# Kernel optimization log

Measured on AMD Instinct MI355X. Metric: run time of the kernel, lower is better.

Reference implementation:

```python
import jax, jax.numpy as jnp
import numpy as np

EPS = 1e-5

def _conv3x3(x, w, b):
    # x: (B,C,H,W), w: (O,I,3,3) OIHW, SAME padding, stride 1
    y = jax.lax.conv_general_dilated(x, w, (1, 1), 'SAME',
                                     dimension_numbers=('NCHW', 'OIHW', 'NCHW'))
    return y + b[None, :, None, None]

def _inorm(x):
    # InstanceNorm2d (affine=False, eval-free): per-sample per-channel over HW
    m = jnp.mean(x, axis=(2, 3), keepdims=True)
    v = jnp.var(x, axis=(2, 3), keepdims=True)
    return (x - m) * jax.lax.rsqrt(v + EPS)

def _pac_conv_transpose(x, guide, w, b, stride=2, padding=1, out_pad=1):
    # PacConvTranspose2d (gaussian kernel, not channel-wise, unnormalized):
    # 1) zero-stuff input by stride, pad by (k-1)-padding (+output_padding on the
    #    bottom/right), 2) run a 3x3 conv whose taps are modulated per-pixel by
    #    K_ij = exp(-0.5 * ||g(p+ij) - g(p)||^2) computed from the guidance map.
    # w: (Cin, Cout, k, k)  (torch transposed-conv layout)
    k = w.shape[2]
    B, C, H, Wd = x.shape
    xs = jnp.zeros((B, C, (H - 1) * stride + 1, (Wd - 1) * stride + 1), x.dtype)
    xs = xs.at[:, :, ::stride, ::stride].set(x)
    p = (k - 1) - padding
    xp = jnp.pad(xs, ((0, 0), (0, 0), (p, p + out_pad), (p, p + out_pad)))
    gpad = (k - 1) // 2
    gp = jnp.pad(guide, ((0, 0), (0, 0), (gpad, gpad), (gpad, gpad)))
    Ho, Wo = guide.shape[2], guide.shape[3]
    out = jnp.zeros((B, w.shape[1], Ho, Wo), x.dtype)
    for i in range(k):          # fixed 3x3 tap loop (not a data-dim loop)
        for j in range(k):
            gn = gp[:, :, i:i + Ho, j:j + Wo]
            kk = jnp.exp(-0.5 * jnp.sum((gn - guide) ** 2, axis=1, keepdims=True))  # (B,1,Ho,Wo)
            xn = xp[:, :, i:i + Ho, j:j + Wo]                                        # (B,Cin,Ho,Wo)
            out = out + jnp.einsum('bchw,co->bohw', xn * kk, w[:, :, i, j])
    return out + b[None, :, None, None]

def setup_inputs() -> dict:
    key = jax.random.key(0)
    ks = jax.random.split(key, 16)
    C = 64
    s = 0.02  # small weight scale to keep gaussian adaptive kernels well-conditioned
    inp = {
        'x':      jax.random.normal(ks[0], (1, 4 * C, 64, 64), jnp.float32),
        'ef_lv2': jax.random.normal(ks[1], (1, 2 * C, 128, 128), jnp.float32),
        'ef_lv1': jax.random.normal(ks[2], (1, C, 256, 256), jnp.float32),
        'w_adj2': jax.random.normal(ks[3], (4 * C, 2 * C, 3, 3), jnp.float32) * s,
        'b_adj2': jnp.zeros((4 * C,), jnp.float32),
        'w_adj1': jax.random.normal(ks[4], (2 * C, C, 3, 3), jnp.float32) * s,
        'b_adj1': jnp.zeros((2 * C,), jnp.float32),
        'w_pac16': jax.random.normal(ks[5], (4 * C, 2 * C, 3, 3), jnp.float32) * s,
        'b_pac16': jnp.zeros((2 * C,), jnp.float32),
        'w_pac20': jax.random.normal(ks[6], (2 * C, C, 3, 3), jnp.float32) * s,
        'b_pac20': jnp.zeros((C,), jnp.float32),
        'w_out':  jax.random.normal(ks[7], (3, C, 3, 3), jnp.float32) * s,
        'b_out':  jnp.zeros((3,), jnp.float32),
    }
    return inp

def reference(x, ef_lv2, ef_lv1, w_adj2, b_adj2, w_adj1, b_adj1,
              w_pac16, b_pac16, w_pac20, b_pac20, w_out, b_out):
    x = _inorm(x) + x                       # layer13 + residual
    x = _inorm(x) + x                       # layer14 + residual
    g2 = _conv3x3(ef_lv2, w_adj2, b_adj2)   # adjust_ef_lv2_pacconv
    x = _pac_conv_transpose(x, g2, w_pac16, b_pac16)  # layer16: 64->128
    x = _inorm(x) + x                       # layer17
    x = _inorm(x) + x                       # layer18
    g1 = _conv3x3(ef_lv1, w_adj1, b_adj1)   # adjust_ef_lv1_pacconv
    x = _pac_conv_transpose(x, g1, w_pac20, b_pac20)  # layer20: 128->256
    x = _inorm(x) + x                       # layer21
    x = _inorm(x) + x                       # layer22
    return _conv3x3(x, w_out, b_out)        # layer24 -> (B,3,256,256)
```

## Files before the change

### kernel.cpp

```cpp
#include <hip/hip_runtime.h>
#include <hip/hip_bf16.h>
#include <cstdint>
#include <cstddef>

#define EPS_IN 1e-5f

typedef __attribute__((ext_vector_type(8))) short short8;
typedef __attribute__((ext_vector_type(4))) float floatx4;
typedef __attribute__((ext_vector_type(8))) unsigned short ushort8;
typedef __attribute__((ext_vector_type(4))) unsigned short ushort4v;
typedef __attribute__((ext_vector_type(4))) unsigned int uint4v;
typedef __attribute__((address_space(3))) unsigned int lds_uint;
typedef __attribute__((address_space(1))) const unsigned int glb_uint;

__device__ __forceinline__ unsigned short f2bf(float f) {
    unsigned int u = __float_as_uint(f);
    u += 0x7FFFu + ((u >> 16) & 1u);
    return (unsigned short)(u >> 16);
}
__device__ __forceinline__ float bf2f(unsigned short s) {
    return __uint_as_float((unsigned int)s << 16);
}
__device__ __forceinline__ float bflo(unsigned int u) {
    return __uint_as_float(u << 16);
}
__device__ __forceinline__ float bfhi(unsigned int u) {
    return __uint_as_float(u & 0xFFFF0000u);
}

__device__ __forceinline__ void composed_norm(float s, float q, float HW,
                                              float& A, float& B) {
    float m1 = s / HW;
    float v1 = q / HW - m1 * m1;
    float r1 = rsqrtf(v1 + EPS_IN);
    float a1 = 1.f + r1;
    float b1 = -m1 * r1;
    float r2 = rsqrtf(a1 * a1 * v1 + EPS_IN);
    float a2 = 1.f + r2;
    A = a1 * a2;
    B = a2 * b1 - m1 * r2;
}

__global__ void zero4_kernel(uint4v* __restrict__ p, long n4) {
    long i = (long)blockIdx.x * blockDim.x + threadIdx.x;
    long stride = (long)gridDim.x * blockDim.x;
    uint4v z = {0u, 0u, 0u, 0u};
    for (; i < n4; i += stride) p[i] = z;
}

__global__ void zero_border_kernel(unsigned short* __restrict__ buf, int C, int H, int W) {
    int Hp = H + 2, Wp = W + 2;
    int nb = 2 * Wp + 2 * H;
    int cg8 = C >> 3;
    int idx = blockIdx.x * blockDim.x + threadIdx.x;
    if (idx >= nb * cg8) return;
    int cg = idx % cg8;
    int bi = idx / cg8;
    int y, x;
    if (bi < Wp) { y = 0; x = bi; }
    else if (bi < 2 * Wp) { y = Hp - 1; x = bi - Wp; }
    else {
        int k = bi - 2 * Wp;
        y = 1 + (k >> 1);
        x = (k & 1) ? (Wp - 1) : 0;
    }
    ushort8 z = {0, 0, 0, 0, 0, 0, 0, 0};
    *(ushort8*)&buf[((size_t)y * Wp + x) * C + cg * 8] = z;
}

__global__ void pad_convert_kernel(const float* __restrict__ in, unsigned short* __restrict__ xp,
                                   int C, int H, int W) {
    int HW = H * W;
    int t = blockIdx.x * blockDim.x + threadIdx.x;
    int p = t % HW;
    int cg = t / HW;
    int y = p / W, x = p % W;
    ushort8 v;
#pragma unroll
    for (int i = 0; i < 8; i++)
        v[i] = f2bf(in[(size_t)(cg * 8 + i) * HW + p]);
    *(ushort8*)&xp[((size_t)(y + 1) * (W + 2) + (x + 1)) * C + cg * 8] = v;
}

__global__ void reorder_w_kernel(const float* __restrict__ w, unsigned short* __restrict__ wre,
                                 int O, int C) {
    int cg8 = C >> 3;
    int t = blockIdx.x * blockDim.x + threadIdx.x;
    int cg = t % cg8;
    int o = (t / cg8) % O;
    int tap = t / (cg8 * O);
    if (tap >= 9) return;
    ushort8 v;
#pragma unroll
    for (int i = 0; i < 8; i++)
        v[i] = f2bf(w[((size_t)o * C + cg * 8 + i) * 9 + tap]);
    *(ushort8*)&wre[((size_t)tap * O + o) * C + cg * 8] = v;
}

template <int CIN>
__launch_bounds__(256, 2)
__global__ void conv3x3_mfma_kernel(const unsigned short* __restrict__ xp,
                                    const unsigned short* __restrict__ wre,
                                    const float* __restrict__ bias,
                                    unsigned short* __restrict__ gpl,
                                    int O, int H, int W) {
    __shared__ short Bbuf[390 * 32];
    __shared__ short Abuf[3 * 128 * 32];
    int tid = threadIdx.x;
    int lane = tid & 63, wid = tid >> 6;
    int mi = wid >> 1, ni = wid & 1;
    int l15 = lane & 15, khi = lane >> 4;
    int tpr = W >> 7;
    int y = blockIdx.x / tpr;
    int x0 = (blockIdx.x % tpr) << 7;
    int o0 = blockIdx.y << 7;
    int Wp = W + 2;
    int HW = H * W;

    floatx4 acc[4][4];
#pragma unroll
    for (int sm = 0; sm < 4; sm++)
#pragma unroll
        for (int r = 0; r < 4; r++) {
            float bv = bias[o0 + mi * 64 + sm * 16 + khi * 4 + r];
#pragma unroll
            for (int sn = 0; sn < 4; sn++) acc[sm][sn][r] = bv;
        }

    for (int cc = 0; cc < CIN / 32; cc++) {
        __syncthreads();
#pragma unroll
        for (int k = 0; k < 7; k++) {
            int s = k * 256 + tid;
            if (s < 1560) {
                int r = s >> 2, q = s & 3;
                int dy = r / 130, col = r % 130;
                const unsigned short* g =
                    xp + ((size_t)(y + dy) * Wp + x0 + col) * CIN + cc * 32 + q * 8;
                __builtin_amdgcn_global_load_lds((glb_uint*)g, (lds_uint*)(Bbuf + s * 8), 16, 0, 0);
            }
        }
        for (int dy = 0; dy < 3; dy++) {
            __syncthreads();
#pragma unroll
            for (int k = 0; k < 6; k++) {
                int s = k * 256 + tid;
                int dx = s >> 9, m = (s >> 2) & 127, q = s & 3;
                const unsigned short* g =
                    wre + ((size_t)((dy * 3 + dx) * O + o0 + m)) * CIN + cc * 32 + q * 8;
                __builtin_amdgcn_global_load_lds((glb_uint*)g, (lds_uint*)(Abuf + s * 8), 16, 0, 0);
            }
            __syncthreads();
#pragma unroll
            for (int dx = 0; dx < 3; dx++) {
                short8 a[4], b[4];
#pragma unroll
                for (int sm = 0; sm < 4; sm++)
                    a[sm] = *(const short8*)&Abuf[(dx * 128 + mi * 64 + sm * 16 + l15) * 32 + khi * 8];
#pragma unroll
                for (int sn = 0; sn < 4; sn++)
                    b[sn] = *(const short8*)&Bbuf[(dy * 130 + ni * 64 + sn * 16 + l15 + dx) * 32 + khi * 8];
#pragma unroll
                for (int sm = 0; sm < 4; sm++)
#pragma unroll
                    for (int sn = 0; sn < 4; sn++)
                        acc[sm][sn] = __builtin_amdgcn_mfma_f32_16x16x32_bf16(
                            a[sm], b[sn], acc[sm][sn], 0, 0, 0);
            }
        }
    }
#pragma unroll
    for (int sm = 0; sm < 4; sm++)
#pragma unroll
        for (int sn = 0; sn < 4; sn++) {
            int ob = o0 + mi * 64 + sm * 16 + khi * 4;
            int px = x0 + ni * 64 + sn * 16 + l15;
#pragma unroll
            for (int r = 0; r < 4; r++)
                gpl[(size_t)(ob + r) * HW + (size_t)y * W + px] = f2bf(acc[sm][sn][r]);
        }
}

template <int CIN>
__launch_bounds__(256, 1)
__global__ void conv3x3_mfma_at_kernel(const unsigned short* __restrict__ xp,
                                       const unsigned short* __restrict__ wre,
                                       const float* __restrict__ bias,
                                       unsigned short* __restrict__ gpl,
                                       int O, int H, int W) {
    __shared__ short Bbuf[390 * 32];
    __shared__ short Abuf[9 * 128 * 32];
    int tid = threadIdx.x;
    int lane = tid & 63, wid = tid >> 6;
    int mi = wid >> 1, ni = wid & 1;
    int l15 = lane & 15, khi = lane >> 4;
    int tpr = W >> 7;
    int y = blockIdx.x / tpr;
    int x0 = (blockIdx.x % tpr) << 7;
    int o0 = blockIdx.y << 7;
    int Wp = W + 2;
    int HW = H * W;

    floatx4 acc[4][4];
#pragma unroll
    for (int sm = 0; sm < 4; sm++)
#pragma unroll
        for (int r = 0; r < 4; r++) {
            float bv = bias[o0 + mi * 64 + sm * 16 + khi * 4 + r];
#pragma unroll
            for (int sn = 0; sn < 4; sn++) acc[sm][sn][r] = bv;
        }

    for (int cc = 0; cc < CIN / 32; cc++) {
        __syncthreads();
#pragma unroll
        for (int k = 0; k < 7; k++) {
            int s = k * 256 + tid;
            if (s < 1560) {
                int r = s >> 2, q = s & 3;
                int dy = r / 130, col = r % 130;
                const unsigned short* g =
                    xp + ((size_t)(y + dy) * Wp + x0 + col) * CIN + cc * 32 + q * 8;
                __builtin_amdgcn_global_load_lds((glb_uint*)g, (lds_uint*)(Bbuf + s * 8), 16, 0, 0);
            }
        }
#pragma unroll
        for (int k = 0; k < 18; k++) {
            int s = k * 256 + tid;
            int row = s >> 2, q = s & 3;
            int tap = row >> 7, m = row & 127;
            const unsigned short* g =
                wre + ((size_t)(tap * O + o0 + m)) * CIN + cc * 32 + q * 8;
            __builtin_amdgcn_global_load_lds((glb_uint*)g, (lds_uint*)(Abuf + s * 8), 16, 0, 0);
        }
        __syncthreads();
#pragma unroll
        for (int dy = 0; dy < 3; dy++)
#pragma unroll
            for (int dx = 0; dx < 3; dx++) {
                short8 a[4], b[4];
#pragma unroll
                for (int sm = 0; sm < 4; sm++)
                    a[sm] = *(const short8*)&Abuf[((dy * 3 + dx) * 128 + mi * 64 + sm * 16 + l15) * 32 + khi * 8];
#pragma unroll
                for (int sn = 0; sn < 4; sn++)
                    b[sn] = *(const short8*)&Bbuf[(dy * 130 + ni * 64 + sn * 16 + l15 + dx) * 32 + khi * 8];
#pragma unroll
                for (int sm = 0; sm < 4; sm++)
#pragma unroll
                    for (int sn = 0; sn < 4; sn++)
                        acc[sm][sn] = __builtin_amdgcn_mfma_f32_16x16x32_bf16(
                            a[sm], b[sn], acc[sm][sn], 0, 0, 0);
            }
    }
#pragma unroll
    for (int sm = 0; sm < 4; sm++)
#pragma unroll
        for (int sn = 0; sn < 4; sn++) {
            int ob = o0 + mi * 64 + sm * 16 + khi * 4;
            int px = x0 + ni * 64 + sn * 16 + l15;
#pragma unroll
            for (int r = 0; r < 4; r++)
                gpl[(size_t)(ob + r) * HW + (size_t)y * W + px] = f2bf(acc[sm][sn][r]);
        }
}

template <int CC>
__global__ void kk_planar_part_kernel(const unsigned short* __restrict__ g,
                                      float* __restrict__ Sp,
                                      int H, int W) {
    int Wh = W >> 1;
    int idx = blockIdx.x * blockDim.x + threadIdx.x;
    int y = idx / Wh, xs = idx % Wh;
    int HW = H * W, HW4 = HW >> 2;
    int ys = y >> 1, ry = y & 1;
    bool xg = (xs + 1 < Wh);
    int off2 = xg ? 1 : 0;
    int c0 = blockIdx.y * CC;
    const unsigned short* gy = g + (size_t)y * W + 2 * xs + (size_t)c0 * HW;
    float* S = Sp + (size_t)blockIdx.y * 9 * HW4;
    int slot = ys * Wh + xs;

    if (ry == 0) {
        float s3 = 0.f, s5 = 0.f;
        for (int c = 0; c < CC; c++) {
            const unsigned int* p = (const unsigned int*)(gy + (size_t)c * HW);
            unsigned int cc = p[0];
            unsigned int n2 = p[off2];
            float ce = bflo(cc), co = bfhi(cc);
            float d3 = ce - co;
            float d5 = bflo(n2) - co;
            s3 += d3 * d3;
            s5 += d5 * d5;
        }
        S[(size_t)3 * HW4 + slot] = s3;
        S[(size_t)4 * HW4 + slot] = 0.f;
        S[(size_t)5 * HW4 + slot] = xg ? s5 : 0.f;
    } else {
        bool yg = (y + 1 < H);
        float s0 = 0.f, s1 = 0.f, s2 = 0.f, s6 = 0.f, s7 = 0.f, s8 = 0.f;
        if (yg) {
            for (int c = 0; c < CC; c++) {
                const unsigned int* pc = (const unsigned int*)(gy + (size_t)c * HW);
                const unsigned int* pm = (const unsigned int*)(gy - W + (size_t)c * HW);
                const unsigned int* pp = (const unsigned int*)(gy + W + (size_t)c * HW);
                unsigned int cc = pc[0];
                unsigned int m0 = pm[0], m2 = pm[off2];
                unsigned int q0 = pp[0], q2 = pp[off2];
                float ce = bflo(cc), co = bfhi(cc);
                float nm = bflo(m0), np = bflo(q0);
                float d1 = nm - ce, d0 = nm - co, d2 = bflo(m2) - co;
                float d7 = np - ce, d6 = np - co, d8 = bflo(q2) - co;
                s1 += d1 * d1; s0 += d0 * d0; s2 += d2 * d2;
                s7 += d7 * d7; s6 += d6 * d6; s8 += d8 * d8;
            }
        } else {
            for (int c = 0; c < CC; c++) {
                const unsigned int* pc = (const unsigned int*)(gy + (size_t)c * HW);
                const unsigned int* pm = (const unsigned int*)(gy - W + (size_t)c * HW);
                unsigned int cc = pc[0];
                unsigned int m0 = pm[0], m2 = pm[off2];
                float ce = bflo(cc), co = bfhi(cc);
                float nm = bflo(m0);
                float d1 = nm - ce, d0 = nm - co, d2 = bflo(m2) - co;
                s1 += d1 * d1; s0 += d0 * d0; s2 += d2 * d2;
            }
        }
        S[(size_t)0 * HW4 + slot] = s0;
        S[(size_t)1 * HW4 + slot] = s1;
        S[(size_t)2 * HW4 + slot] = xg ? s2 : 0.f;
        S[(size_t)6 * HW4 + slot] = s6;
        S[(size_t)7 * HW4 + slot] = s7;
        S[(size_t)8 * HW4 + slot] = (xg && yg) ? s8 : 0.f;
    }
}

__global__ void kk_reduce_kernel(const float* __restrict__ Sp, float* __restrict__ Sf,
                                 int n, int nch) {
    int i = blockIdx.x * blockDim.x + threadIdx.x;
    if (i >= n) return;
    float s = 0.f;
    for (int ch = 0; ch < nch; ch++) s += Sp[(size_t)ch * n + i];
    Sf[i] = s;
}

__global__ void in_stats_kernel(const float* __restrict__ in, float2* __restrict__ part,
                                int HW, int NB) {
    int c = blockIdx.y, bi = blockIdx.x;
    const float* src = in + (size_t)c * HW + (size_t)bi * 4096;
    float s = 0.f, q = 0.f;
#pragma unroll
    for (int k = 0; k < 4; k++) {
        float4 v = *(const float4*)(src + k * 1024 + threadIdx.x * 4);
        s += v.x + v.y + v.z + v.w;
        q += v.x * v.x + v.y * v.y + v.z * v.z + v.w * v.w;
    }
#pragma unroll
    for (int off = 32; off >= 1; off >>= 1) {
        s += __shfl_down(s, off, 64);
        q += __shfl_down(q, off, 64);
    }
    __shared__ float ss[4], sq[4];
    int wave = threadIdx.x >> 6;
    if ((threadIdx.x & 63) == 0) { ss[wave] = s; sq[wave] = q; }
    __syncthreads();
    if (threadIdx.x == 0) {
        float2 o;
        o.x = ss[0] + ss[1] + ss[2] + ss[3];
        o.y = sq[0] + sq[1] + sq[2] + sq[3];
        part[c * NB + bi] = o;
    }
}

__global__ void transpose_norm2_kernel(const float* __restrict__ in,
                                       const float2* __restrict__ parts, int NB,
                                       unsigned short* __restrict__ xt,
                                       int C, int HW) {
    int t = blockIdx.x * blockDim.x + threadIdx.x;
    int p = t % HW;
    int cg = t / HW;
    float Av[8], Bv[8];
#pragma unroll
    for (int i = 0; i < 8; i++) {
        int c = cg * 8 + i;
        float s = 0.f, q = 0.f;
        for (int nb = 0; nb < NB; nb++) {
            float2 pp = parts[c * NB + nb];
            s += pp.x; q += pp.y;
        }
        composed_norm(s, q, (float)HW, Av[i], Bv[i]);
    }
    ushort8 v;
#pragma unroll
    for (int i = 0; i < 8; i++) {
        float x = in[(size_t)(cg * 8 + i) * HW + p];
        v[i] = f2bf(fmaf(x, Av[i], Bv[i]));
    }
    *(ushort8*)&xt[(size_t)p * C + cg * 8] = v;
}

__global__ void stack_w_kernel(const float* __restrict__ w, unsigned short* __restrict__ wst,
                               int C, int O) {
    int cg8 = C >> 3;
    int t = blockIdx.x * blockDim.x + threadIdx.x;
    int cg = t % cg8;
    int o = (t / cg8) % O;
    int tap = t / (cg8 * O);
    if (tap >= 9) return;
    ushort8 v;
#pragma unroll
    for (int i = 0; i < 8; i++)
        v[i] = f2bf(w[((size_t)(cg * 8 + i) * O + o) * 9 + tap]);
    *(ushort8*)&wst[((size_t)tap * O + o) * C + cg * 8] = v;
}

template <int K>
__launch_bounds__(256, 3)
__global__ void gemm_bt_kernel(const unsigned short* __restrict__ A,
                               const unsigned short* __restrict__ B,
                               unsigned short* __restrict__ P, int N) {
    __shared__ short Ab[128 * 32];
    __shared__ short Bb[128 * 32];
    int tid = threadIdx.x;
    int lane = tid & 63, wid = tid >> 6;
    int mi = wid >> 1, ni = wid & 1;
    int l15 = lane & 15, khi = lane >> 4;
    int m0 = blockIdx.y << 7, n0 = blockIdx.x << 7;

    floatx4 acc[4][4];
#pragma unroll
    for (int sm = 0; sm < 4; sm++)
#pragma unroll
        for (int sn = 0; sn < 4; sn++)
#pragma unroll
            for (int r = 0; r < 4; r++) acc[sm][sn][r] = 0.f;

    for (int kc = 0; kc < K / 32; kc++) {
        __syncthreads();
#pragma unroll
        for (int k = 0; k < 2; k++) {
            int s = k * 256 + tid;
            int row = s >> 2, q = s & 3;
            const unsigned short* ga = A + (size_t)(m0 + row) * K + kc * 32 + q * 8;
            __builtin_amdgcn_global_load_lds((glb_uint*)ga, (lds_uint*)(Ab + s * 8), 16, 0, 0);
            const unsigned short* gb = B + (size_t)(n0 + row) * K + kc * 32 + q * 8;
            __builtin_amdgcn_global_load_lds((glb_uint*)gb, (lds_uint*)(Bb + s * 8), 16, 0, 0);
        }
        __syncthreads();
        short8 a[4], b[4];
#pragma unroll
        for (int sm = 0; sm < 4; sm++)
            a[sm] = *(const short8*)&Ab[(mi * 64 + sm * 16 + l15) * 32 + khi * 8];
#pragma unroll
        for (int sn = 0; sn < 4; sn++)
            b[sn] = *(const short8*)&Bb[(ni * 64 + sn * 16 + l15) * 32 + khi * 8];
#pragma unroll
        for (int sm = 0; sm < 4; sm++)
#pragma unroll
            for (int sn = 0; sn < 4; sn++)
                acc[sm][sn] = __builtin_amdgcn_mfma_f32_16x16x32_bf16(
                    a[sm], b[sn], acc[sm][sn], 0, 0, 0);
    }
#pragma unroll
    for (int sm = 0; sm < 4; sm++)
#pragma unroll
        for (int sn = 0; sn < 4; sn++) {
            int m = m0 + mi * 64 + sm * 16 + khi * 4;
            int n = n0 + ni * 64 + sn * 16 + l15;
#pragma unroll
            for (int r = 0; r < 4; r++)
                P[(size_t)(m + r) * N + n] = f2bf(acc[sm][sn][r]);
        }
}

__global__ void pac_combine2_kernel(const unsigned short* __restrict__ P,
                                    const float* __restrict__ S,
                                    const float* __restrict__ bias,
                                    float* __restrict__ out,
                                    float2* __restrict__ statOut,
                                    int O, int Hi, int Wi) {
    int HW4 = Hi * Wi;
    int Wo = Wi * 2;
    int HoWo = 4 * HW4;
    int idx = blockIdx.x * blockDim.x + threadIdx.x;
    int pixh = idx % HW4;
    int og = idx / HW4;
    int ys = pixh / Wi, xs = pixh % Wi;
    int ry = blockIdx.z;
    int y = 2 * ys + ry;
    bool xg = (xs + 1 < Wi);
    bool yg = (ys + 1 < Hi);
    size_t rowb = (size_t)ys * Wi + xs;

    float ev[4], ov[4];

    if (ry == 0) {
        float k3 = __expf(-0.5f * S[(size_t)3 * HW4 + pixh]);
        float k4 = __expf(-0.5f * S[(size_t)4 * HW4 + pixh]);
        float k5 = __expf(-0.5f * S[(size_t)5 * HW4 + pixh]);
#pragma unroll
        for (int r = 0; r < 4; r++) {
            int o = og * 4 + r;
            float bv = bias[o];
            const unsigned short* p3 = P + (size_t)(3 * O + o) * HW4 + rowb;
            const unsigned short* p4 = P + (size_t)(4 * O + o) * HW4 + rowb;
            const unsigned short* p5 = P + (size_t)(5 * O + o) * HW4 + rowb;
            float v4 = bf2f(p4[0]);
            float v3 = bf2f(p3[0]);
            float v5 = xg ? bf2f(p5[1]) : 0.f;
            ev[r] = bv + k4 * v4;
            ov[r] = bv + k3 * v3 + k5 * v5;
        }
    } else {
        float k0 = __expf(-0.5f * S[(size_t)0 * HW4 + pixh]);
        float k1 = __expf(-0.5f * S[(size_t)1 * HW4 + pixh]);
        float k2 = __expf(-0.5f * S[(size_t)2 * HW4 + pixh]);
        float k6 = __expf(-0.5f * S[(size_t)6 * HW4 + pixh]);
        float k7 = __expf(-0.5f * S[(size_t)7 * HW4 + pixh]);
        float k8 = __expf(-0.5f * S[(size_t)8 * HW4 + pixh]);
#pragma unroll
        for (int r = 0; r < 4; r++) {
            int o = og * 4 + r;
            float bv = bias[o];
            const unsigned short* p0 = P + (size_t)(0 * O + o) * HW4 + rowb;
            const unsigned short* p1 = P + (size_t)(1 * O + o) * HW4 + rowb;
            const unsigned short* p2 = P + (size_t)(2 * O + o) * HW4 + rowb;
            const unsigned short* p6 = P + (size_t)(6 * O + o) * HW4 + rowb + Wi;
            const unsigned short* p7 = P + (size_t)(7 * O + o) * HW4 + rowb + Wi;
            const unsigned short* p8 = P + (size_t)(8 * O + o) * HW4 + rowb + Wi;
            float v1 = bf2f(p1[0]);
            float v0 = bf2f(p0[0]);
            float v2 = xg ? bf2f(p2[1]) : 0.f;
            float v7 = yg ? bf2f(p7[0]) : 0.f;
            float v6 = yg ? bf2f(p6[0]) : 0.f;
            float v8 = (yg && xg) ? bf2f(p8[1]) : 0.f;
            ev[r] = bv + k1 * v1 + k7 * v7;
            ov[r] = bv + k0 * v0 + k2 * v2 + k6 * v6 + k8 * v8;
        }
    }
#pragma unroll
    for (int r = 0; r < 4; r++) {
        float2 st; st.x = ev[r]; st.y = ov[r];
        *(float2*)&out[(size_t)(og * 4 + r) * HoWo + (size_t)y * Wo + 2 * xs] = st;
    }

    __shared__ float rs[4][4], rq[4][4];
    int wave = threadIdx.x >> 6;
#pragma unroll
    for (int r = 0; r < 4; r++) {
        float s = ev[r] + ov[r];
        float q = ev[r] * ev[r] + ov[r] * ov[r];
#pragma unroll
        for (int off = 32; off >= 1; off >>= 1) {
            s += __shfl_down(s, off, 64);
            q += __shfl_down(q, off, 64);
        }
        if ((threadIdx.x & 63) == 0) { rs[wave][r] = s; rq[wave][r] = q; }
    }
    __syncthreads();
    if (threadIdx.x < 4) {
        int r = threadIdx.x;
        float s = rs[0][r] + rs[1][r] + rs[2][r] + rs[3][r];
        float q = rq[0][r] + rq[1][r] + rq[2][r] + rq[3][r];
        atomicAdd(&statOut[og * 4 + r].x, s);
        atomicAdd(&statOut[og * 4 + r].y, q);
    }
}

__global__ void conv_part_norm_kernel(const float* __restrict__ in, const float* __restrict__ w,
                                      const float2* __restrict__ parts, int NB,
                                      float* __restrict__ Pf, int H, int W) {
    __shared__ float wsm[16 * 9 * 3];
    __shared__ float am[16], bm[16];
    int q0 = blockIdx.y * 16;
    int HW = H * W;
    for (int t = threadIdx.x; t < 432; t += blockDim.x) {
        int oc = t % 3;
        int tap = (t / 3) % 9;
        int c = t / 27;
        wsm[t] = w[((size_t)oc * 64 + q0 + c) * 9 + tap];
    }
    if (threadIdx.x < 16) {
        int c = q0 + threadIdx.x;
        float s = 0.f, q = 0.f;
        for (int nb = 0; nb < NB; nb++) {
            float2 pp = parts[c * NB + nb];
            s += pp.x; q += pp.y;
        }
        float A, B;
        composed_norm(s, q, (float)HW, A, B);
        am[threadIdx.x] = A;
        bm[threadIdx.x] = B;
    }
    __syncthreads();
    int pix = blockIdx.x * blockDim.x + threadIdx.x;
    int y = pix / W, x = pix % W;
    float acc[3] = {0.f, 0.f, 0.f};
    bool xl = (x > 0), xr = (x < W - 1);
    for (int c = 0; c < 16; c++) {
        const float* base = in + (size_t)(q0 + c) * HW + pix;
        const float* wc = wsm + c * 27;
        float ac = am[c], bc = bm[c];
#pragma unroll
        for (int dy = 0; dy < 3; dy++) {
            int yy = y + dy - 1;
            if (yy < 0 || yy >= H) continue;
            const float* row = base + (dy - 1) * W;
            float v0 = xl ? fmaf(row[-1], ac, bc) : 0.f;
            float v1 = fmaf(row[0], ac, bc);
            float v2 = xr ? fmaf(row[1], ac, bc) : 0.f;
#pragma unroll
            for (int ob = 0; ob < 3; ob++) {
                acc[ob] += v0 * wc[(dy * 3 + 0) * 3 + ob];
                acc[ob] += v1 * wc[(dy * 3 + 1) * 3 + ob];
                acc[ob] += v2 * wc[(dy * 3 + 2) * 3 + ob];
            }
        }
    }
#pragma unroll
    for (int ob = 0; ob < 3; ob++)
        Pf[(size_t)(blockIdx.y * 3 + ob) * HW + pix] = acc[ob];
}

__global__ void conv_fin_kernel(const float* __restrict__ Pf, const float* __restrict__ bias,
                                float* __restrict__ out, int HW) {
    int pix = blockIdx.x * blockDim.x + threadIdx.x;
#pragma unroll
    for (int ob = 0; ob < 3; ob++) {
        float a = bias[ob];
#pragma unroll
        for (int q = 0; q < 4; q++)
            a += Pf[(size_t)(q * 3 + ob) * HW + pix];
        out[(size_t)ob * HW + pix] = a;
    }
}

extern "C" void kernel_launch(void* const* d_in, const int* in_sizes, int n_in,
                              void* d_out, int out_size, void* d_ws, size_t ws_size,
                              hipStream_t stream) {
    const float* x      = (const float*)d_in[0];
    const float* ef2    = (const float*)d_in[1];
    const float* ef1    = (const float*)d_in[2];
    const float* w_adj2 = (const float*)d_in[3];
    const float* b_adj2 = (const float*)d_in[4];
    const float* w_adj1 = (const float*)d_in[5];
    const float* b_adj1 = (const float*)d_in[6];
    const float* w_p16  = (const float*)d_in[7];
    const float* b_p16  = (const float*)d_in[8];
    const float* w_p20  = (const float*)d_in[9];
    const float* b_p20  = (const float*)d_in[10];
    const float* w_out  = (const float*)d_in[11];
    const float* b_out  = (const float*)d_in[12];
    float* out = (float*)d_out;

    float* ws = (float*)d_ws;
    float* bx1 = ws + 1048576;
    float* bx2 = ws + 3145728;
    float* bk2c = ws + 7340032;
    float* bk1c = ws + 7376896;
    float2* statX   = (float2*)(ws + 7524352);
    float2* statP16 = (float2*)(ws + 7525376);
    float2* statP20 = (float2*)(ws + 7526656);
    unsigned short* Wt20 = (unsigned short*)(ws + 7528832);
    unsigned short* Gp1  = (unsigned short*)(ws + 7569792);
    unsigned short* P16  = (unsigned short*)(ws + 7569792);
    unsigned short* Xt16 = (unsigned short*)(ws + 9929088);
    unsigned short* Wt16 = (unsigned short*)(ws + 10453376);
    unsigned short* P20  = (unsigned short*)(ws + 7569792);
    unsigned short* Gp2  = (unsigned short*)(ws + 12812672);
    unsigned short* Xt20 = (unsigned short*)(ws + 12812672);
    unsigned short* Xp2 = (unsigned short*)(ws + 14975872);
    unsigned short* Wr2 = (unsigned short*)(ws + 16057472);
    unsigned short* Xp1 = (unsigned short*)(ws + 16204928);
    unsigned short* Wr1 = (unsigned short*)(ws + 18334976);
    float* Pf = ws + 14975872;
    float* Sp2 = ws + 18371840;
    float* Sp1 = ws + 18961664;

    zero4_kernel<<<2, 256, 0, stream>>>((uint4v*)(ws + 7524352), 4480 / 4);
    zero_border_kernel<<<33, 256, 0, stream>>>(Xp2, 128, 128, 128);
    zero_border_kernel<<<33, 256, 0, stream>>>(Xp1, 64, 256, 256);

    pad_convert_kernel<<<1024, 256, 0, stream>>>(ef2, Xp2, 128, 128, 128);
    reorder_w_kernel<<<144, 256, 0, stream>>>(w_adj2, Wr2, 256, 128);
    conv3x3_mfma_at_kernel<128><<<dim3(128, 2), 256, 0, stream>>>(Xp2, Wr2, b_adj2, Gp2, 256, 128, 128);
    kk_planar_part_kernel<16><<<dim3(32, 16), 256, 0, stream>>>(Gp2, Sp2, 128, 128);
    kk_reduce_kernel<<<144, 256, 0, stream>>>(Sp2, bk2c, 36864, 16);

    pad_convert_kernel<<<2048, 256, 0, stream>>>(ef1, Xp1, 64, 256, 256);
    reorder_w_kernel<<<36, 256, 0, stream>>>(w_adj1, Wr1, 128, 64);
    conv3x3_mfma_kernel<64><<<dim3(512, 1), 256, 0, stream>>>(Xp1, Wr1, b_adj1, Gp1, 128, 256, 256);
    kk_planar_part_kernel<16><<<dim3(128, 8), 256, 0, stream>>>(Gp1, Sp1, 256, 256);
    kk_reduce_kernel<<<576, 256, 0, stream>>>(Sp1, bk1c, 147456, 8);

    in_stats_kernel<<<dim3(1, 256), 256, 0, stream>>>(x, statX, 4096, 1);
    transpose_norm2_kernel<<<512, 256, 0, stream>>>(x, statX, 1, Xt16, 256, 4096);

    stack_w_kernel<<<144, 256, 0, stream>>>(w_p16, Wt16, 256, 128);
    gemm_bt_kernel<256><<<dim3(32, 9), 256, 0, stream>>>(Wt16, Xt16, P16, 4096);
    pac_combine2_kernel<<<dim3(512, 1, 2), 256, 0, stream>>>(P16, bk2c, b_p16, bx1, statP16, 128, 64, 64);

    transpose_norm2_kernel<<<1024, 256, 0, stream>>>(bx1, statP16, 1, Xt20, 128, 16384);

    stack_w_kernel<<<36, 256, 0, stream>>>(w_p20, Wt20, 128, 64);
    gemm_bt_kernel<128><<<dim3(128, 5), 256, 0, stream>>>(Wt20, Xt20, P20, 16384);
    pac_combine2_kernel<<<dim3(1024, 1, 2), 256, 0, stream>>>(P20, bk1c, b_p20, bx2, statP20, 64, 128, 128);

    conv_part_norm_kernel<<<dim3(256, 4), 256, 0, stream>>>(bx2, w_out, statP20, 1, Pf, 256, 256);
    conv_fin_kernel<<<256, 256, 0, stream>>>(Pf, b_out, out, 65536);
}
```

Baseline: 276.6 us.

## Store intermediate activations in bf16 and merge prep kernels into fewer launches

The PAC combine outputs are now written as bf16 instead of fp32. The downstream transpose-norm and final conv kernels read bf16, which halves the traffic on the two largest intermediate buffers. Border zeroing, stat clearing and all four weight reorders are folded into two launches, cutting launch overhead. This costs precision in the intermediate activations, while the norm statistics are still computed from fp32 values.

After: 264.6 us. -4.3%, faster.

```diff
diff --git a/kernel.cpp b/kernel.cpp
--- a/kernel.cpp
+++ b/kernel.cpp
@@ -41,19 +41,9 @@
     B = a2 * b1 - m1 * r2;
 }
 
-__global__ void zero4_kernel(uint4v* __restrict__ p, long n4) {
-    long i = (long)blockIdx.x * blockDim.x + threadIdx.x;
-    long stride = (long)gridDim.x * blockDim.x;
-    uint4v z = {0u, 0u, 0u, 0u};
-    for (; i < n4; i += stride) p[i] = z;
-}
-
-__global__ void zero_border_kernel(unsigned short* __restrict__ buf, int C, int H, int W) {
+__device__ __forceinline__ void border_zero(unsigned short* buf, int C, int H, int W, int idx) {
     int Hp = H + 2, Wp = W + 2;
-    int nb = 2 * Wp + 2 * H;
     int cg8 = C >> 3;
-    int idx = blockIdx.x * blockDim.x + threadIdx.x;
-    if (idx >= nb * cg8) return;
     int cg = idx % cg8;
     int bi = idx / cg8;
     int y, x;
@@ -68,6 +58,58 @@
     *(ushort8*)&buf[((size_t)y * Wp + x) * C + cg * 8] = z;
 }
 
+__global__ void init_kernel(uint4v* __restrict__ statz, int n4,
+                            unsigned short* __restrict__ xp2,
+                            unsigned short* __restrict__ xp1) {
+    int t = blockIdx.x * blockDim.x + threadIdx.x;
+    const int N2 = 516 * 16;
+    const int N1 = 1028 * 8;
+    if (t < n4) {
+        uint4v z = {0u, 0u, 0u, 0u};
+        statz[t] = z;
+    } else if (t < n4 + N2) {
+        border_zero(xp2, 128, 128, 128, t - n4);
+    } else if (t < n4 + N2 + N1) {
+        border_zero(xp1, 64, 256, 256, t - n4 - N2);
+    }
+}
+
+__device__ __forceinline__ void reorder_one(const float* w, unsigned short* dst,
+                                            int O, int C, int j) {
+    int cg8 = C >> 3;
+    int cg = j % cg8;
+    int o = (j / cg8) % O;
+    int tap = j / (cg8 * O);
+    ushort8 v;
+#pragma unroll
+    for (int i = 0; i < 8; i++)
+        v[i] = f2bf(w[((size_t)o * C + cg * 8 + i) * 9 + tap]);
+    *(ushort8*)&dst[((size_t)tap * O + o) * C + cg * 8] = v;
+}
+__device__ __forceinline__ void stack_one(const float* w, unsigned short* dst,
+                                          int C, int O, int j) {
+    int cg8 = C >> 3;
+    int cg = j % cg8;
+    int o = (j / cg8) % O;
+    int tap = j / (cg8 * O);
+    ushort8 v;
+#pragma unroll
+    for (int i = 0; i < 8; i++)
+        v[i] = f2bf(w[((size_t)(cg * 8 + i) * O + o) * 9 + tap]);
+    *(ushort8*)&dst[((size_t)tap * O + o) * C + cg * 8] = v;
+}
+
+__global__ void prep_w_kernel(const float* __restrict__ w_adj2, unsigned short* __restrict__ Wr2,
+                              const float* __restrict__ w_adj1, unsigned short* __restrict__ Wr1,
+                              const float* __restrict__ w_p16, unsigned short* __restrict__ Wt16,
+                              const float* __restrict__ w_p20, unsigned short* __restrict__ Wt20) {
+    int t = blockIdx.x * blockDim.x + threadIdx.x;
+    if (t < 36864) reorder_one(w_adj2, Wr2, 256, 128, t);
+    else if (t < 46080) reorder_one(w_adj1, Wr1, 128, 64, t - 36864);
+    else if (t < 82944) stack_one(w_p16, Wt16, 256, 128, t - 46080);
+    else if (t < 92160) stack_one(w_p20, Wt20, 128, 64, t - 82944);
+}
+
 __global__ void pad_convert_kernel(const float* __restrict__ in, unsigned short* __restrict__ xp,
                                    int C, int H, int W) {
     int HW = H * W;
@@ -80,21 +122,6 @@
     for (int i = 0; i < 8; i++)
         v[i] = f2bf(in[(size_t)(cg * 8 + i) * HW + p]);
     *(ushort8*)&xp[((size_t)(y + 1) * (W + 2) + (x + 1)) * C + cg * 8] = v;
-}
-
-__global__ void reorder_w_kernel(const float* __restrict__ w, unsigned short* __restrict__ wre,
-                                 int O, int C) {
-    int cg8 = C >> 3;
-    int t = blockIdx.x * blockDim.x + threadIdx.x;
-    int cg = t % cg8;
-    int o = (t / cg8) % O;
-    int tap = t / (cg8 * O);
-    if (tap >= 9) return;
-    ushort8 v;
-#pragma unroll
-    for (int i = 0; i < 8; i++)
-        v[i] = f2bf(w[((size_t)o * C + cg * 8 + i) * 9 + tap]);
-    *(ushort8*)&wre[((size_t)tap * O + o) * C + cg * 8] = v;
 }
 
 template <int CIN>
@@ -399,19 +426,31 @@
     *(ushort8*)&xt[(size_t)p * C + cg * 8] = v;
 }
 
-__global__ void stack_w_kernel(const float* __restrict__ w, unsigned short* __restrict__ wst,
-                               int C, int O) {
-    int cg8 = C >> 3;
+__global__ void transpose_norm2_bf16_kernel(const unsigned short* __restrict__ in,
+                                            const float2* __restrict__ parts, int NB,
+                                            unsigned short* __restrict__ xt,
+                                            int C, int HW) {
     int t = blockIdx.x * blockDim.x + threadIdx.x;
-    int cg = t % cg8;
-    int o = (t / cg8) % O;
-    int tap = t / (cg8 * O);
-    if (tap >= 9) return;
+    int p = t % HW;
+    int cg = t / HW;
+    float Av[8], Bv[8];
+#pragma unroll
+    for (int i = 0; i < 8; i++) {
+        int c = cg * 8 + i;
+        float s = 0.f, q = 0.f;
+        for (int nb = 0; nb < NB; nb++) {
+            float2 pp = parts[c * NB + nb];
+            s += pp.x; q += pp.y;
+        }
+        composed_norm(s, q, (float)HW, Av[i], Bv[i]);
+    }
     ushort8 v;
 #pragma unroll
-    for (int i = 0; i < 8; i++)
-        v[i] = f2bf(w[((size_t)(cg * 8 + i) * O + o) * 9 + tap]);
-    *(ushort8*)&wst[((size_t)tap * O + o) * C + cg * 8] = v;
+    for (int i = 0; i < 8; i++) {
+        float x = bf2f(in[(size_t)(cg * 8 + i) * HW + p]);
+        v[i] = f2bf(fmaf(x, Av[i], Bv[i]));
+    }
+    *(ushort8*)&xt[(size_t)p * C + cg * 8] = v;
 }
 
 template <int K>
@@ -476,7 +515,7 @@
 __global__ void pac_combine2_kernel(const unsigned short* __restrict__ P,
                                     const float* __restrict__ S,
                                     const float* __restrict__ bias,
-                                    float* __restrict__ out,
+                                    unsigned short* __restrict__ out,
                                     float2* __restrict__ statOut,
                                     int O, int Hi, int Wi) {
     int HW4 = Hi * Wi;
@@ -540,8 +579,8 @@
     }
 #pragma unroll
     for (int r = 0; r < 4; r++) {
-        float2 st; st.x = ev[r]; st.y = ov[r];
-        *(float2*)&out[(size_t)(og * 4 + r) * HoWo + (size_t)y * Wo + 2 * xs] = st;
+        unsigned int pk = (unsigned int)f2bf(ev[r]) | ((unsigned int)f2bf(ov[r]) << 16);
+        *(unsigned int*)&out[(size_t)(og * 4 + r) * HoWo + (size_t)y * Wo + 2 * xs] = pk;
     }
 
     __shared__ float rs[4][4], rq[4][4];
@@ -567,7 +606,8 @@
     }
 }
 
-__global__ void conv_part_norm_kernel(const float* __restrict__ in, const float* __restrict__ w,
+__global__ void conv_part_norm_kernel(const unsigned short* __restrict__ in,
+                                      const float* __restrict__ w,
                                       const float2* __restrict__ parts, int NB,
                                       float* __restrict__ Pf, int H, int W) {
     __shared__ float wsm[16 * 9 * 3];
@@ -598,17 +638,17 @@
     float acc[3] = {0.f, 0.f, 0.f};
     bool xl = (x > 0), xr = (x < W - 1);
     for (int c = 0; c < 16; c++) {
-        const float* base = in + (size_t)(q0 + c) * HW + pix;
+        const unsigned short* base = in + (size_t)(q0 + c) * HW + pix;
         const float* wc = wsm + c * 27;
         float ac = am[c], bc = bm[c];
 #pragma unroll
         for (int dy = 0; dy < 3; dy++) {
             int yy = y + dy - 1;
             if (yy < 0 || yy >= H) continue;
-            const float* row = base + (dy - 1) * W;
-            float v0 = xl ? fmaf(row[-1], ac, bc) : 0.f;
-            float v1 = fmaf(row[0], ac, bc);
-            float v2 = xr ? fmaf(row[1], ac, bc) : 0.f;
+            const unsigned short* row = base + (dy - 1) * W;
+            float v0 = xl ? fmaf(bf2f(row[-1]), ac, bc) : 0.f;
+            float v1 = fmaf(bf2f(row[0]), ac, bc);
+            float v2 = xr ? fmaf(bf2f(row[1]), ac, bc) : 0.f;
 #pragma unroll
             for (int ob = 0; ob < 3; ob++) {
                 acc[ob] += v0 * wc[(dy * 3 + 0) * 3 + ob];
@@ -654,8 +694,9 @@
     float* out = (float*)d_out;
 
     float* ws = (float*)d_ws;
-    float* bx1 = ws + 1048576;
-    float* bx2 = ws + 3145728;
+    unsigned short* bxb1 = (unsigned short*)(ws + 1048576);
+    unsigned short* bxb2 = (unsigned short*)(ws + 3145728);
+    unsigned short* Wt16 = (unsigned short*)(ws + 5242880);
     float* bk2c = ws + 7340032;
     float* bk1c = ws + 7376896;
     float2* statX   = (float2*)(ws + 7524352);
@@ -665,7 +706,6 @@
     unsigned short* Gp1  = (unsigned short*)(ws + 7569792);
     unsigned short* P16  = (unsigned short*)(ws + 7569792);
     unsigned short* Xt16 = (unsigned short*)(ws + 9929088);
-    unsigned short* Wt16 = (unsigned short*)(ws + 10453376);
     unsigned short* P20  = (unsigned short*)(ws + 7569792);
     unsigned short* Gp2  = (unsigned short*)(ws + 12812672);
     unsigned short* Xt20 = (unsigned short*)(ws + 12812672);
@@ -677,18 +717,15 @@
     float* Sp2 = ws + 18371840;
     float* Sp1 = ws + 18961664;
 
-    zero4_kernel<<<2, 256, 0, stream>>>((uint4v*)(ws + 7524352), 4480 / 4);
-    zero_border_kernel<<<33, 256, 0, stream>>>(Xp2, 128, 128, 128);
-    zero_border_kernel<<<33, 256, 0, stream>>>(Xp1, 64, 256, 256);
+    init_kernel<<<69, 256, 0, stream>>>((uint4v*)(ws + 7524352), 1120, Xp2, Xp1);
+    prep_w_kernel<<<360, 256, 0, stream>>>(w_adj2, Wr2, w_adj1, Wr1, w_p16, Wt16, w_p20, Wt20);
 
     pad_convert_kernel<<<1024, 256, 0, stream>>>(ef2, Xp2, 128, 128, 128);
-    reorder_w_kernel<<<144, 256, 0, stream>>>(w_adj2, Wr2, 256, 128);
     conv3x3_mfma_at_kernel<128><<<dim3(128, 2), 256, 0, stream>>>(Xp2, Wr2, b_adj2, Gp2, 256, 128, 128);
     kk_planar_part_kernel<16><<<dim3(32, 16), 256, 0, stream>>>(Gp2, Sp2, 128, 128);
     kk_reduce_kernel<<<144, 256, 0, stream>>>(Sp2, bk2c, 36864, 16);
 
     pad_convert_kernel<<<2048, 256, 0, stream>>>(ef1, Xp1, 64, 256, 256);
-    reorder_w_kernel<<<36, 256, 0, stream>>>(w_adj1, Wr1, 128, 64);
     conv3x3_mfma_kernel<64><<<dim3(512, 1), 256, 0, stream>>>(Xp1, Wr1, b_adj1, Gp1, 128, 256, 256);
     kk_planar_part_kernel<16><<<dim3(128, 8), 256, 0, stream>>>(Gp1, Sp1, 256, 256);
     kk_reduce_kernel<<<576, 256, 0, stream>>>(Sp1, bk1c, 147456, 8);
@@ -696,16 +733,14 @@
     in_stats_kernel<<<dim3(1, 256), 256, 0, stream>>>(x, statX, 4096, 1);
     transpose_norm2_kernel<<<512, 256, 0, stream>>>(x, statX, 1, Xt16, 256, 4096);
 
-    stack_w_kernel<<<144, 256, 0, stream>>>(w_p16, Wt16, 256, 128);
     gemm_bt_kernel<256><<<dim3(32, 9), 256, 0, stream>>>(Wt16, Xt16, P16, 4096);
-    pac_combine2_kernel<<<dim3(512, 1, 2), 256, 0, stream>>>(P16, bk2c, b_p16, bx1, statP16, 128, 64, 64);
-
-    transpose_norm2_kernel<<<1024, 256, 0, stream>>>(bx1, statP16, 1, Xt20, 128, 16384);
-
-    stack_w_kernel<<<36, 256, 0, stream>>>(w_p20, Wt20, 128, 64);
+    pac_combine2_kernel<<<dim3(512, 1, 2), 256, 0, stream>>>(P16, bk2c, b_p16, bxb1, statP16, 128, 64, 64);
+
+    transpose_norm2_bf16_kernel<<<1024, 256, 0, stream>>>(bxb1, statP16, 1, Xt20, 128, 16384);
+
     gemm_bt_kernel<128><<<dim3(128, 5), 256, 0, stream>>>(Wt20, Xt20, P20, 16384);
-    pac_combine2_kernel<<<dim3(1024, 1, 2), 256, 0, stream>>>(P20, bk1c, b_p20, bx2, statP20, 64, 128, 128);
-
-    conv_part_norm_kernel<<<dim3(256, 4), 256, 0, stream>>>(bx2, w_out, statP20, 1, Pf, 256, 256);
+    pac_combine2_kernel<<<dim3(1024, 1, 2), 256, 0, stream>>>(P20, bk1c, b_p20, bxb2, statP20, 64, 128, 128);
+
+    conv_part_norm_kernel<<<dim3(256, 4), 256, 0, stream>>>(bxb2, w_out, statP20, 1, Pf, 256, 256);
     conv_fin_kernel<<<256, 256, 0, stream>>>(Pf, b_out, out, 65536);
 }
```
